# Kernel optimization log

Hardware: AMD Instinct MI355X
Metric: run time of the kernel (lower is better)

The kernel has to match this reference:

```python
import jax, jax.numpy as jnp
import numpy as np

B, C, H, W = 512, 256, 16, 16
K = H * W          # 256, hardcoded in the original reshape((1, 256))
N_CLASSES = 2      # binary private attribute
SIGMA = 1.0


def setup_inputs() -> dict:
    key = jax.random.key(0)
    k1, k2 = jax.random.split(key)
    mu = jax.random.normal(k1, (B, C, H, W), dtype=jnp.float32)
    private_attribute = jax.random.randint(k2, (B,), 0, N_CLASSES)
    cov = jnp.eye(K, dtype=jnp.float32) * SIGMA  # module buffer: eye(256) * sigma
    return {"mu": mu, "cov": cov, "private_attribute": private_attribute}


def reference(mu, cov, private_attribute):
    x = mu.reshape(B, C, K)                       # (B, C, 256)
    labels = private_attribute                    # (B,) int
    ones = jnp.ones((B,), x.dtype)
    counts = jax.ops.segment_sum(ones, labels, num_segments=N_CLASSES)        # (L,)
    safe = jnp.maximum(counts, 1.0)
    means = jax.ops.segment_sum(x, labels, num_segments=N_CLASSES) \
            / safe[:, None, None]                 # (L, C, K) per-label mean
    centered = x - means[labels]                  # (B, C, K) x_i - mu_{label(i)}
    onehot = (labels[:, None] == jnp.arange(N_CLASSES)[None, :]).astype(x.dtype)  # (B, L)
    # per-label scatter matrices: Sigma_l = sum_{i: label=l} (x_i-mu_l)^T (x_i-mu_l)
    S = jnp.stack([
        jnp.einsum('bci,bcj->cij', centered * onehot[:, l][:, None, None], centered)
        for l in range(N_CLASSES)
    ])                                            # (L, C, K, K)
    Sigma = cov[None, None] + S / safe[:, None, None, None]
    Sinv = jnp.linalg.inv(Sigma)                  # (L, C, K, K)
    _, logdet = jnp.linalg.slogdet(Sigma)         # (L, C)
    result = jnp.zeros((), x.dtype)
    # pairwise KL(N_i || N_j) with the original's asymmetric index pattern
    for i in range(N_CLASSES - 1):
        for j in range(1, N_CLASSES):
            if j == i:
                continue
            tr = jnp.einsum('cab,cba->c', Sinv[j], Sigma[i])         # trace(S2^{-1} S1)
            d = means[j] - means[i]                                  # (C, K)
            quad = jnp.einsum('ci,cij,cj->c', d, Sinv[j], d)
            kl = 0.5 * (tr + quad - K + logdet[j] - logdet[i])       # (C,)
            result = result + jnp.sum(kl) * counts[i] * counts[j]
    return result / C / (B ** 2)
```

## Files before the change

kernel.cpp:

```cpp
#include <hip/hip_runtime.h>
#include <cmath>

typedef __attribute__((ext_vector_type(4))) float f32x4;
typedef __attribute__((ext_vector_type(8))) short bf16x8;

#define MSZ 65536

__device__ __forceinline__ unsigned short f2bf(float f){
  unsigned u = __float_as_uint(f);
  unsigned r = (u + 0x7FFFu + ((u >> 16) & 1u)) >> 16;
  return (unsigned short)r;
}

__device__ __forceinline__ float dot4(f32x4 a, f32x4 b){
  return a.x*b.x + a.y*b.y + a.z*b.z + a.w*b.w;
}

__device__ __forceinline__ void tri_decode(int i, int& R, int& C){
  int Rv = (int)((sqrtf(8.f*(float)i + 1.f) - 1.f) * 0.5f);
  while ((Rv+1)*(Rv+2)/2 <= i) ++Rv;
  while (Rv*(Rv+1)/2 > i) --Rv;
  R = Rv; C = i - Rv*(Rv+1)/2;
}

__global__ void k_sentinel(float* __restrict__ out){ out[0] = 123456.0f; }

__global__ void k0_partition(const int* __restrict__ lab, int* __restrict__ cnt, int* __restrict__ idx){
  __shared__ int lcnt0[8], lcnt1[8];
  int t = threadIdx.x;
  int w = t >> 6, lane = t & 63;
  int l = lab[t];
  unsigned long long m0 = __ballot(l == 0);
  unsigned long long bm = (lane == 0) ? 0ull : ((1ull << lane) - 1ull);
  int r0 = __popcll(m0 & bm);
  int r1 = __popcll((~m0) & bm);
  if (lane == 0){ lcnt0[w] = __popcll(m0); lcnt1[w] = 64 - __popcll(m0); }
  __syncthreads();
  int base0 = 0, base1 = 0, n0 = 0;
  #pragma unroll
  for (int i = 0; i < 8; ++i){
    if (i < w){ base0 += lcnt0[i]; base1 += lcnt1[i]; }
    n0 += lcnt0[i];
  }
  int pos = (l == 0) ? (base0 + r0) : (n0 + base1 + r1);
  idx[pos] = t;
  if (t == 0){ cnt[0] = n0; cnt[1] = 512 - n0; }
}

__global__ __launch_bounds__(1024) void k1_means(const float* __restrict__ x, const int* __restrict__ lab,
                                                 const int* __restrict__ cnt, float* __restrict__ means){
  __shared__ int labs[512];
  __shared__ float part[8][256];
  int t = threadIdx.x, c = blockIdx.x;
  if (t < 512) labs[t] = lab[t];
  __syncthreads();
  int k = t & 255, bq = t >> 8;
  float s0 = 0.f, s1 = 0.f;
  const float* xc = x + (size_t)c * 256 + k;
  for (int b = bq; b < 512; b += 4){
    float v = xc[(size_t)b * 65536];
    if (labs[b] == 0) s0 += v; else s1 += v;
  }
  part[bq*2+0][k] = s0;
  part[bq*2+1][k] = s1;
  __syncthreads();
  if (t < 256){
    float m0 = part[0][t] + part[2][t] + part[4][t] + part[6][t];
    float m1 = part[1][t] + part[3][t] + part[5][t] + part[7][t];
    float n0 = (float)cnt[0], n1 = (float)cnt[1];
    means[(size_t)c * 256 + t]         = m0 / fmaxf(n0, 1.f);
    means[(size_t)(256 + c) * 256 + t] = m1 / fmaxf(n1, 1.f);
  }
}

__global__ __launch_bounds__(512) void k2_gram(const float* __restrict__ x, const float* __restrict__ cov,
    const float* __restrict__ means, const int* __restrict__ cnt, const int* __restrict__ idx,
    float* __restrict__ sig, int c0){
  __shared__ uint4 XT4[1280];
  __shared__ float mlds[256];
  int t = threadIdx.x;
  int bid = blockIdx.x;
  int l = bid & 1, c = c0 + (bid >> 1);
  int n0 = cnt[0], n1 = cnt[1];
  int n = l ? n1 : n0;
  int start = l ? n0 : 0;
  if (t < 256) mlds[t] = means[(size_t)(l * 256 + c) * 256 + t];

  f32x4 acc[8][4];
  #pragma unroll
  for (int i = 0; i < 8; ++i)
    #pragma unroll
    for (int jn = 0; jn < 4; ++jn){ f32x4 z; z.x = 0.f; z.y = 0.f; z.z = 0.f; z.w = 0.f; acc[i][jn] = z; }

  int lane = t & 63, wav = t >> 6;
  int wr = wav >> 2, wc = wav & 3;
  int lrow = lane & 15, lhalf = lane >> 4;
  int kq = t & 255, bh = t >> 8;
  int nst = (n + 31) >> 5;

  for (int s = 0; s < nst; ++s){
    __syncthreads();
    unsigned pk[8];
    #pragma unroll
    for (int m = 0; m < 8; ++m){
      int b0 = s * 32 + bh * 16 + 2 * m;
      float v0 = 0.f, v1 = 0.f;
      if (b0 < n)     v0 = x[((size_t)idx[start + b0] * 256 + c) * 256 + kq];
      if (b0 + 1 < n) v1 = x[((size_t)idx[start + b0 + 1] * 256 + c) * 256 + kq];
      pk[m] = (unsigned)f2bf(v0) | ((unsigned)f2bf(v1) << 16);
    }
    XT4[kq * 5 + bh * 2 + 0] = make_uint4(pk[0], pk[1], pk[2], pk[3]);
    XT4[kq * 5 + bh * 2 + 1] = make_uint4(pk[4], pk[5], pk[6], pk[7]);
    __syncthreads();
    bf16x8 af[8], bfr[4];
    #pragma unroll
    for (int i = 0; i < 8; ++i){
      int T = wr * 8 + i;
      af[i] = *reinterpret_cast<const bf16x8*>(&XT4[(T * 16 + lrow) * 5 + lhalf]);
    }
    #pragma unroll
    for (int jn = 0; jn < 4; ++jn){
      int T = wc * 4 + jn;
      bfr[jn] = *reinterpret_cast<const bf16x8*>(&XT4[(T * 16 + lrow) * 5 + lhalf]);
    }
    #pragma unroll
    for (int i = 0; i < 8; ++i)
      #pragma unroll
      for (int jn = 0; jn < 4; ++jn)
        acc[i][jn] = __builtin_amdgcn_mfma_f32_16x16x32_bf16(af[i], bfr[jn], acc[i][jn], 0, 0, 0);
  }
  __syncthreads();

  float invn = 1.0f / fmaxf((float)n, 1.0f);
  float* sigm = sig + (size_t)bid * MSZ;
  #pragma unroll
  for (int i = 0; i < 8; ++i){
    int Rb = (wr * 8 + i) * 16 + lhalf * 4;
    #pragma unroll
    for (int jn = 0; jn < 4; ++jn){
      int Cc = (wc * 4 + jn) * 16 + lrow;
      #pragma unroll
      for (int r = 0; r < 4; ++r){
        int R = Rb + r;
        float v = acc[i][jn][r] * invn + cov[R * 256 + Cc] - mlds[R] * mlds[Cc];
        sigm[R * 256 + Cc] = (Cc <= R) ? v : 0.0f;
      }
    }
  }
}

__device__ void factor128_v13(float* __restrict__ LB, int t, float& ldacc){
  for (int kb = 0; kb < 4; ++kb){
    int j0 = kb * 32;
    if (t < 64){
      #pragma unroll 1
      for (int s8 = 0; s8 < 8; ++s8){
        int js = j0 + 4*s8;
        float a00 = LB[(js+0)*132 + js+0];
        float a10 = LB[(js+1)*132 + js+0], a11 = LB[(js+1)*132 + js+1];
        float a20 = LB[(js+2)*132 + js+0], a21 = LB[(js+2)*132 + js+1], a22 = LB[(js+2)*132 + js+2];
        float a30 = LB[(js+3)*132 + js+0], a31 = LB[(js+3)*132 + js+1], a32 = LB[(js+3)*132 + js+2], a33 = LB[(js+3)*132 + js+3];
        float l00 = sqrtf(a00);
        float i00 = 1.0f / l00;
        float l10 = a10 * i00, l20 = a20 * i00, l30 = a30 * i00;
        float l11 = sqrtf(a11 - l10*l10);
        float i11 = 1.0f / l11;
        float l21 = (a21 - l20*l10) * i11, l31 = (a31 - l30*l10) * i11;
        float l22 = sqrtf(a22 - l20*l20 - l21*l21);
        float i22 = 1.0f / l22;
        float l32 = (a32 - l30*l20 - l31*l21) * i22;
        float l33 = sqrtf(a33 - l30*l30 - l31*l31 - l32*l32);
        float i33 = 1.0f / l33;
        if (t == 0){
          LB[(js+0)*132 + js+0] = l00;
          LB[(js+1)*132 + js+0] = l10; LB[(js+1)*132 + js+1] = l11;
          LB[(js+2)*132 + js+0] = l20; LB[(js+2)*132 + js+1] = l21; LB[(js+2)*132 + js+2] = l22;
          LB[(js+3)*132 + js+0] = l30; LB[(js+3)*132 + js+1] = l31; LB[(js+3)*132 + js+2] = l32; LB[(js+3)*132 + js+3] = l33;
          ldacc += logf(l00) + logf(l11) + logf(l22) + logf(l33);
        }
        int cnt2 = 28 - 4*s8;
        int r = js + 4 + t;
        if (t < cnt2){
          float w0 = LB[r*132 + js+0], w1 = LB[r*132 + js+1], w2 = LB[r*132 + js+2], w3 = LB[r*132 + js+3];
          w0 = w0 * i00;
          w1 = (w1 - l10*w0) * i11;
          w2 = (w2 - l20*w0 - l21*w1) * i22;
          w3 = (w3 - l30*w0 - l31*w1 - l32*w2) * i33;
          LB[r*132 + js+0] = w0; LB[r*132 + js+1] = w1; LB[r*132 + js+2] = w2; LB[r*132 + js+3] = w3;
          #pragma unroll 4
          for (int cq2 = js + 4; cq2 <= r; ++cq2){
            f32x4 Lc = *(const f32x4*)&LB[cq2*132 + js];
            LB[r*132 + cq2] -= w0*Lc.x + w1*Lc.y + w2*Lc.z + w3*Lc.w;
          }
        }
      }
    }
    __syncthreads();
    int nr = 96 - j0;
    if (nr > 0){
      if (t < nr){
        int row = j0 + 32 + t;
        float w[32];
        #pragma unroll
        for (int q = 0; q < 8; ++q){
          f32x4 v = *(const f32x4*)&LB[row*132 + j0 + 4*q];
          w[4*q] = v.x; w[4*q+1] = v.y; w[4*q+2] = v.z; w[4*q+3] = v.w;
        }
        #pragma unroll
        for (int cc = 0; cc < 32; ++cc){
          float s = w[cc];
          #pragma unroll
          for (int p = 0; p < cc; ++p) s -= LB[(j0+cc)*132 + j0 + p] * w[p];
          w[cc] = s / LB[(j0+cc)*132 + j0 + cc];
        }
        #pragma unroll
        for (int q = 0; q < 8; ++q){
          f32x4 v; v.x = w[4*q]; v.y = w[4*q+1]; v.z = w[4*q+2]; v.w = w[4*q+3];
          *(f32x4*)&LB[row*132 + j0 + 4*q] = v;
        }
      }
      __syncthreads();
      int nt = nr >> 2;
      int Tt = nt*(nt+1)/2;
      if (t < Tt){
        int R, C; tri_decode(t, R, C);
        int rb = j0+32+4*R, cb = j0+32+4*C;
        float s[16];
        #pragma unroll
        for (int q = 0; q < 16; ++q) s[q] = 0.f;
        #pragma unroll 4
        for (int qc = 0; qc < 8; ++qc){
          f32x4 a0 = *(const f32x4*)&LB[(rb+0)*132 + j0 + 4*qc];
          f32x4 a1 = *(const f32x4*)&LB[(rb+1)*132 + j0 + 4*qc];
          f32x4 a2 = *(const f32x4*)&LB[(rb+2)*132 + j0 + 4*qc];
          f32x4 a3 = *(const f32x4*)&LB[(rb+3)*132 + j0 + 4*qc];
          f32x4 b0 = *(const f32x4*)&LB[(cb+0)*132 + j0 + 4*qc];
          f32x4 b1 = *(const f32x4*)&LB[(cb+1)*132 + j0 + 4*qc];
          f32x4 b2 = *(const f32x4*)&LB[(cb+2)*132 + j0 + 4*qc];
          f32x4 b3 = *(const f32x4*)&LB[(cb+3)*132 + j0 + 4*qc];
          s[0]+=dot4(a0,b0);  s[1]+=dot4(a0,b1);  s[2]+=dot4(a0,b2);  s[3]+=dot4(a0,b3);
          s[4]+=dot4(a1,b0);  s[5]+=dot4(a1,b1);  s[6]+=dot4(a1,b2);  s[7]+=dot4(a1,b3);
          s[8]+=dot4(a2,b0);  s[9]+=dot4(a2,b1);  s[10]+=dot4(a2,b2); s[11]+=dot4(a2,b3);
          s[12]+=dot4(a3,b0); s[13]+=dot4(a3,b1); s[14]+=dot4(a3,b2); s[15]+=dot4(a3,b3);
        }
        #pragma unroll
        for (int i2 = 0; i2 < 4; ++i2)
          #pragma unroll
          for (int jl = 0; jl < 4; ++jl)
            LB[(rb+i2)*132 + cb+jl] -= s[i2*4+jl];
      }
    }
    __syncthreads();
  }
}

__global__ __launch_bounds__(512) void k3a_chol(float* __restrict__ sig, float* __restrict__ logdet, int c0){
  extern __shared__ float smem[];
  float* LB = smem;
  float* LT = smem + 16896;
  int t = threadIdx.x;
  int bid = blockIdx.x;
  int l = bid & 1, c = c0 + (bid >> 1);
  float* A = sig + (size_t)bid * MSZ;
  float ldacc = 0.f;

  for (int i = t; i < 4096; i += 512){
    int r = i >> 5, q = i & 31;
    *(f32x4*)&LB[r*132 + 4*q] = *(const f32x4*)&A[(size_t)r*256 + 4*q];
  }
  __syncthreads();
  factor128_v13(LB, t, ldacc);
  for (int i = t; i < 4096; i += 512){
    int r = i >> 5, q = i & 31;
    f32x4 v = *(const f32x4*)&LB[r*132 + 4*q];
    int cb = 4*q;
    v.x = (cb+0 <= r) ? v.x : 0.f;
    v.y = (cb+1 <= r) ? v.y : 0.f;
    v.z = (cb+2 <= r) ? v.z : 0.f;
    v.w = (cb+3 <= r) ? v.w : 0.f;
    *(f32x4*)&A[(size_t)r*256 + 4*q] = v;
  }
  __syncthreads();

  {
    int r2 = t >> 2, g = t & 3;
    for (int kb = 0; kb < 4; ++kb){
      f32x4 v0 = *(const f32x4*)&A[(size_t)(128+r2)*256 + 32*kb + 8*g];
      f32x4 v1 = *(const f32x4*)&A[(size_t)(128+r2)*256 + 32*kb + 8*g + 4];
      float accv[8] = {v0.x, v0.y, v0.z, v0.w, v1.x, v1.y, v1.z, v1.w};
      for (int p = 0; p < kb; ++p){
        __syncthreads();
        for (int i = t; i < 1024; i += 512){
          int j = i & 31, q = i >> 5;
          LT[q*33 + j] = A[(size_t)(32*kb + j)*256 + 32*p + q];
        }
        __syncthreads();
        f32x4 wv[8];
        #pragma unroll
        for (int q = 0; q < 8; ++q) wv[q] = *(const f32x4*)&LB[r2*132 + 32*p + 4*q];
        #pragma unroll
        for (int q4 = 0; q4 < 8; ++q4)
          #pragma unroll
          for (int jl = 0; jl < 8; ++jl)
            accv[jl] -= wv[q4].x * LT[(4*q4+0)*33 + 8*g+jl]
                      + wv[q4].y * LT[(4*q4+1)*33 + 8*g+jl]
                      + wv[q4].z * LT[(4*q4+2)*33 + 8*g+jl]
                      + wv[q4].w * LT[(4*q4+3)*33 + 8*g+jl];
      }
      #pragma unroll
      for (int jl = 0; jl < 8; ++jl) LB[r2*132 + 32*kb + 8*g + jl] = accv[jl];
      __syncthreads();
      for (int i = t; i < 1024; i += 512){
        int cc = i >> 5, p = i & 31;
        LT[cc*33 + p] = A[(size_t)(32*kb + cc)*256 + 32*kb + p];
      }
      __syncthreads();
      if (t < 128){
        float w[32];
        #pragma unroll
        for (int q = 0; q < 8; ++q){
          f32x4 v = *(const f32x4*)&LB[t*132 + 32*kb + 4*q];
          w[4*q] = v.x; w[4*q+1] = v.y; w[4*q+2] = v.z; w[4*q+3] = v.w;
        }
        #pragma unroll
        for (int cc = 0; cc < 32; ++cc){
          float s = w[cc];
          #pragma unroll
          for (int p = 0; p < cc; ++p) s -= LT[cc*33 + p] * w[p];
          w[cc] = s / LT[cc*33 + cc];
        }
        #pragma unroll
        for (int q = 0; q < 8; ++q){
          f32x4 v; v.x = w[4*q]; v.y = w[4*q+1]; v.z = w[4*q+2]; v.w = w[4*q+3];
          *(f32x4*)&LB[t*132 + 32*kb + 4*q] = v;
        }
      }
      __syncthreads();
    }
    for (int i = t; i < 4096; i += 512){
      int rr = i >> 5, q = i & 31;
      *(f32x4*)&A[(size_t)(128+rr)*256 + 4*q] = *(const f32x4*)&LB[rr*132 + 4*q];
    }
  }

  float s1[16], s2[16];
  int R1 = 0, C1 = 0, R2 = 0, C2 = 0;
  bool v1 = (t < 528), v2 = (t < 16);
  if (v1) tri_decode(t, R1, C1);
  if (v2) tri_decode(512 + t, R2, C2);
  #pragma unroll
  for (int q = 0; q < 16; ++q){ s1[q] = 0.f; s2[q] = 0.f; }
  if (v1){
    for (int qc = 0; qc < 32; ++qc){
      f32x4 a0 = *(const f32x4*)&LB[(4*R1+0)*132 + 4*qc];
      f32x4 a1 = *(const f32x4*)&LB[(4*R1+1)*132 + 4*qc];
      f32x4 a2 = *(const f32x4*)&LB[(4*R1+2)*132 + 4*qc];
      f32x4 a3 = *(const f32x4*)&LB[(4*R1+3)*132 + 4*qc];
      f32x4 b0 = *(const f32x4*)&LB[(4*C1+0)*132 + 4*qc];
      f32x4 b1 = *(const f32x4*)&LB[(4*C1+1)*132 + 4*qc];
      f32x4 b2 = *(const f32x4*)&LB[(4*C1+2)*132 + 4*qc];
      f32x4 b3 = *(const f32x4*)&LB[(4*C1+3)*132 + 4*qc];
      s1[0]+=dot4(a0,b0);  s1[1]+=dot4(a0,b1);  s1[2]+=dot4(a0,b2);  s1[3]+=dot4(a0,b3);
      s1[4]+=dot4(a1,b0);  s1[5]+=dot4(a1,b1);  s1[6]+=dot4(a1,b2);  s1[7]+=dot4(a1,b3);
      s1[8]+=dot4(a2,b0);  s1[9]+=dot4(a2,b1);  s1[10]+=dot4(a2,b2); s1[11]+=dot4(a2,b3);
      s1[12]+=dot4(a3,b0); s1[13]+=dot4(a3,b1); s1[14]+=dot4(a3,b2); s1[15]+=dot4(a3,b3);
    }
    #pragma unroll
    for (int i2 = 0; i2 < 4; ++i2){
      f32x4 av = *(const f32x4*)&A[(size_t)(128+4*R1+i2)*256 + 128 + 4*C1];
      s1[i2*4+0] = av.x - s1[i2*4+0];
      s1[i2*4+1] = av.y - s1[i2*4+1];
      s1[i2*4+2] = av.z - s1[i2*4+2];
      s1[i2*4+3] = av.w - s1[i2*4+3];
    }
  }
  if (v2){
    for (int qc = 0; qc < 32; ++qc){
      f32x4 a0 = *(const f32x4*)&LB[(4*R2+0)*132 + 4*qc];
      f32x4 a1 = *(const f32x4*)&LB[(4*R2+1)*132 + 4*qc];
      f32x4 a2 = *(const f32x4*)&LB[(4*R2+2)*132 + 4*qc];
      f32x4 a3 = *(const f32x4*)&LB[(4*R2+3)*132 + 4*qc];
      f32x4 b0 = *(const f32x4*)&LB[(4*C2+0)*132 + 4*qc];
      f32x4 b1 = *(const f32x4*)&LB[(4*C2+1)*132 + 4*qc];
      f32x4 b2 = *(const f32x4*)&LB[(4*C2+2)*132 + 4*qc];
      f32x4 b3 = *(const f32x4*)&LB[(4*C2+3)*132 + 4*qc];
      s2[0]+=dot4(a0,b0);  s2[1]+=dot4(a0,b1);  s2[2]+=dot4(a0,b2);  s2[3]+=dot4(a0,b3);
      s2[4]+=dot4(a1,b0);  s2[5]+=dot4(a1,b1);  s2[6]+=dot4(a1,b2);  s2[7]+=dot4(a1,b3);
      s2[8]+=dot4(a2,b0);  s2[9]+=dot4(a2,b1);  s2[10]+=dot4(a2,b2); s2[11]+=dot4(a2,b3);
      s2[12]+=dot4(a3,b0); s2[13]+=dot4(a3,b1); s2[14]+=dot4(a3,b2); s2[15]+=dot4(a3,b3);
    }
    #pragma unroll
    for (int i2 = 0; i2 < 4; ++i2){
      f32x4 av = *(const f32x4*)&A[(size_t)(128+4*R2+i2)*256 + 128 + 4*C2];
      s2[i2*4+0] = av.x - s2[i2*4+0];
      s2[i2*4+1] = av.y - s2[i2*4+1];
      s2[i2*4+2] = av.z - s2[i2*4+2];
      s2[i2*4+3] = av.w - s2[i2*4+3];
    }
  }
  __syncthreads();
  if (v1){
    #pragma unroll
    for (int i2 = 0; i2 < 4; ++i2)
      #pragma unroll
      for (int jl = 0; jl < 4; ++jl)
        LB[(4*R1+i2)*132 + 4*C1+jl] = s1[i2*4+jl];
  }
  if (v2){
    #pragma unroll
    for (int i2 = 0; i2 < 4; ++i2)
      #pragma unroll
      for (int jl = 0; jl < 4; ++jl)
        LB[(4*R2+i2)*132 + 4*C2+jl] = s2[i2*4+jl];
  }
  __syncthreads();

  factor128_v13(LB, t, ldacc);
  for (int i = t; i < 4096; i += 512){
    int r = i >> 5, q = i & 31;
    f32x4 v = *(const f32x4*)&LB[r*132 + 4*q];
    int cb = 4*q;
    v.x = (cb+0 <= r) ? v.x : 0.f;
    v.y = (cb+1 <= r) ? v.y : 0.f;
    v.z = (cb+2 <= r) ? v.z : 0.f;
    v.w = (cb+3 <= r) ? v.w : 0.f;
    *(f32x4*)&A[(size_t)(128+r)*256 + 128 + 4*q] = v;
  }
  if (t < 32){
    float v = ldacc;
    #pragma unroll
    for (int m = 1; m < 32; m <<= 1) v += __shfl_xor(v, m);
    if (t == 0) logdet[l * 256 + c] = 2.0f * v;
  }
}

__global__ __launch_bounds__(256) void k3b_trsm(float* __restrict__ sig, float* __restrict__ trp, int c0){
  __shared__ float L1blk[32 * 256];
  __shared__ float redw[4];
  int t = threadIdx.x, b = blockIdx.x;
  int lane = t & 63, wav = t >> 6;
  const float* L1 = sig + (size_t)(b * 2 + 1) * MSZ;
  float* W = sig + (size_t)(b * 2) * MSZ;
  float tracc = 0.f;

  for (int RB = 0; RB < 8; ++RB){
    int r0 = RB * 32;
    __syncthreads();
    for (int i = t; i < 32 * 256; i += 256)
      L1blk[i] = L1[(size_t)(r0 + (i >> 8)) * 256 + (i & 255)];
    __syncthreads();

    float acc[32];
    #pragma unroll
    for (int r = 0; r < 32; ++r) acc[r] = W[(size_t)(r0 + r) * 256 + t];

    for (int p = 0; p < r0; p += 8){
      float wv[8];
      #pragma unroll
      for (int q = 0; q < 8; ++q) wv[q] = W[(size_t)(p + q) * 256 + t];
      #pragma unroll
      for (int r = 0; r < 32; ++r){
        const f32x4 La = *(const f32x4*)&L1blk[r * 256 + p];
        const f32x4 Lb = *(const f32x4*)&L1blk[r * 256 + p + 4];
        acc[r] -= La.x * wv[0] + La.y * wv[1] + La.z * wv[2] + La.w * wv[3]
                + Lb.x * wv[4] + Lb.y * wv[5] + Lb.z * wv[6] + Lb.w * wv[7];
      }
    }
    #pragma unroll
    for (int rr = 0; rr < 32; ++rr){
      float v = acc[rr];
      #pragma unroll
      for (int q = 0; q < rr; ++q)
        v -= L1blk[rr * 256 + r0 + q] * acc[q];
      v /= L1blk[rr * 256 + r0 + rr];
      acc[rr] = v;
      tracc += v * v;
      W[(size_t)(r0 + rr) * 256 + t] = v;
    }
  }
  #pragma unroll
  for (int m = 1; m < 64; m <<= 1) tracc += __shfl_xor(tracc, m);
  if (lane == 0) redw[wav] = tracc;
  __syncthreads();
  if (t == 0) trp[c0 + b] = redw[0] + redw[1] + redw[2] + redw[3];
}

__global__ __launch_bounds__(64) void k3c_quad(const float* __restrict__ means, const float* __restrict__ sig,
    const float* __restrict__ trp, const float* __restrict__ logdet, float* __restrict__ klp, int c0){
  __shared__ float y[256];
  int t = threadIdx.x, b = blockIdx.x;
  int c = c0 + b;
  const float* L1 = sig + (size_t)(b * 2 + 1) * MSZ;
  const float* m1p = means + (size_t)(256 + c) * 256;
  const float* m0p = means + (size_t)c * 256;

  for (int r = 0; r < 256; ++r){
    float part = 0.f;
    for (int p = t; p < r; p += 64)
      part += L1[(size_t)r * 256 + p] * y[p];
    #pragma unroll
    for (int m = 1; m < 64; m <<= 1) part += __shfl_xor(part, m);
    if (t == 0)
      y[r] = ((m1p[r] - m0p[r]) - part) / L1[(size_t)r * 256 + r];
    __syncthreads();
  }
  float q = 0.f;
  #pragma unroll
  for (int i = 0; i < 4; ++i){ float v = y[t + 64 * i]; q += v * v; }
  #pragma unroll
  for (int m = 1; m < 64; m <<= 1) q += __shfl_xor(q, m);
  if (t == 0)
    klp[c] = 0.5f * (trp[c] + q - 256.0f + logdet[256 + c] - logdet[c]);
}

__global__ void k4_final(const float* __restrict__ klp, const int* __restrict__ cnt, float* __restrict__ out){
  __shared__ float red[256];
  int t = threadIdx.x;
  red[t] = klp[t];
  __syncthreads();
  for (int s = 128; s > 0; s >>= 1){
    if (t < s) red[t] += red[t + s];
    __syncthreads();
  }
  if (t == 0){
    float n0 = (float)cnt[0], n1 = (float)cnt[1];
    out[0] = red[0] * n0 * n1 / 256.0f / 512.0f / 512.0f;
  }
}

extern "C" void kernel_launch(void* const* d_in, const int* in_sizes, int n_in,
                              void* d_out, int out_size, void* d_ws, size_t ws_size,
                              hipStream_t stream){
  (void)in_sizes; (void)n_in; (void)out_size;
  const float* mu  = (const float*)d_in[0];
  const float* cov = (const float*)d_in[1];
  const int*   lab = (const int*)d_in[2];
  float* out = (float*)d_out;
  char* ws = (char*)d_ws;
  float* means  = (float*)ws;
  float* trp    = (float*)(ws + 524288);
  float* klp    = (float*)(ws + 525312);
  float* logdet = (float*)(ws + 526336);
  int*   cnt    = (int*)  (ws + 528384);
  int*   idx    = (int*)  (ws + 528392);
  float* sig    = (float*)(ws + 1048576);
  const size_t base = 1048576;

  int ch = 0;
  if      (ws_size >= base + (size_t)256 * 2 * MSZ * 4) ch = 256;
  else if (ws_size >= base + (size_t)64  * 2 * MSZ * 4) ch = 64;
  else if (ws_size >= base + (size_t)16  * 2 * MSZ * 4) ch = 16;
  else if (ws_size >= base + (size_t)4   * 2 * MSZ * 4) ch = 4;
  else if (ws_size >= base + (size_t)1   * 2 * MSZ * 4) ch = 1;
  if (ch == 0){
    k_sentinel<<<1, 1, 0, stream>>>(out);
    return;
  }

  const int k3a_lds = 17952 * 4;
  (void)hipFuncSetAttribute((const void*)k3a_chol,
                            hipFuncAttributeMaxDynamicSharedMemorySize, k3a_lds);

  k0_partition<<<1, 512, 0, stream>>>(lab, cnt, idx);
  k1_means<<<256, 1024, 0, stream>>>(mu, lab, cnt, means);
  for (int c0 = 0; c0 < 256; c0 += ch){
    k2_gram<<<ch * 2, 512, 0, stream>>>(mu, cov, means, cnt, idx, sig, c0);
    k3a_chol<<<ch * 2, 512, k3a_lds, stream>>>(sig, logdet, c0);
    k3b_trsm<<<ch, 256, 0, stream>>>(sig, trp, c0);
    k3c_quad<<<ch, 64, 0, stream>>>(means, sig, trp, logdet, klp, c0);
  }
  k4_final<<<1, 256, 0, stream>>>(klp, cnt, out);
}
```

Measured before the change: 1.109 ms.

## Fuse quadratic-form triangular solve into TRSM kernel using shared L blocks

Removes the separate k3c_quad kernel. Its forward substitution for the mean difference now runs in wave 0 of k3b_trsm, reusing the L1 row blocks already staged in LDS. The KL term per channel is then computed there. This drops one launch per chunk and the serial global-memory row reads of the old 64-thread quad kernel. In exchange, wave 0 does extra serial work inside each block step, which could lengthen the TRSM critical path.

New measurement: 929.3 us. -16.2%, faster.

```diff
diff --git a/kernel.cpp b/kernel.cpp
--- a/kernel.cpp
+++ b/kernel.cpp
@@ -434,21 +434,43 @@
   }
 }
 
-__global__ __launch_bounds__(256) void k3b_trsm(float* __restrict__ sig, float* __restrict__ trp, int c0){
+__global__ __launch_bounds__(256) void k3b_trsm(const float* __restrict__ means, float* __restrict__ sig,
+    const float* __restrict__ logdet, float* __restrict__ klp, int c0){
   __shared__ float L1blk[32 * 256];
-  __shared__ float redw[4];
+  __shared__ float yl[256];
+  __shared__ float dl[256];
+  __shared__ float redw[4], redq[4];
   int t = threadIdx.x, b = blockIdx.x;
+  int c = c0 + b;
   int lane = t & 63, wav = t >> 6;
   const float* L1 = sig + (size_t)(b * 2 + 1) * MSZ;
   float* W = sig + (size_t)(b * 2) * MSZ;
   float tracc = 0.f;
 
+  if (t < 256){
+    dl[t] = means[(size_t)(256 + c) * 256 + t] - means[(size_t)c * 256 + t];
+    yl[t] = 0.f;
+  }
+
   for (int RB = 0; RB < 8; ++RB){
     int r0 = RB * 32;
     __syncthreads();
     for (int i = t; i < 32 * 256; i += 256)
       L1blk[i] = L1[(size_t)(r0 + (i >> 8)) * 256 + (i & 255)];
     __syncthreads();
+
+    if (wav == 0){
+      for (int rr = 0; rr < 32; ++rr){
+        int r = r0 + rr;
+        const float* row = &L1blk[rr * 256];
+        float part = row[lane] * yl[lane] + row[lane + 64] * yl[lane + 64]
+                   + row[lane + 128] * yl[lane + 128] + row[lane + 192] * yl[lane + 192];
+        #pragma unroll
+        for (int m = 1; m < 64; m <<= 1) part += __shfl_xor(part, m);
+        float val = (dl[r] - part) / row[r];
+        if (lane == 0) yl[r] = val;
+      }
+    }
 
     float acc[32];
     #pragma unroll
@@ -478,39 +500,19 @@
       W[(size_t)(r0 + rr) * 256 + t] = v;
     }
   }
+  __syncthreads();
+  float qv = (t < 256) ? yl[t] * yl[t] : 0.f;
+  #pragma unroll
+  for (int m = 1; m < 64; m <<= 1) qv += __shfl_xor(qv, m);
   #pragma unroll
   for (int m = 1; m < 64; m <<= 1) tracc += __shfl_xor(tracc, m);
-  if (lane == 0) redw[wav] = tracc;
-  __syncthreads();
-  if (t == 0) trp[c0 + b] = redw[0] + redw[1] + redw[2] + redw[3];
-}
-
-__global__ __launch_bounds__(64) void k3c_quad(const float* __restrict__ means, const float* __restrict__ sig,
-    const float* __restrict__ trp, const float* __restrict__ logdet, float* __restrict__ klp, int c0){
-  __shared__ float y[256];
-  int t = threadIdx.x, b = blockIdx.x;
-  int c = c0 + b;
-  const float* L1 = sig + (size_t)(b * 2 + 1) * MSZ;
-  const float* m1p = means + (size_t)(256 + c) * 256;
-  const float* m0p = means + (size_t)c * 256;
-
-  for (int r = 0; r < 256; ++r){
-    float part = 0.f;
-    for (int p = t; p < r; p += 64)
-      part += L1[(size_t)r * 256 + p] * y[p];
-    #pragma unroll
-    for (int m = 1; m < 64; m <<= 1) part += __shfl_xor(part, m);
-    if (t == 0)
-      y[r] = ((m1p[r] - m0p[r]) - part) / L1[(size_t)r * 256 + r];
-    __syncthreads();
-  }
-  float q = 0.f;
-  #pragma unroll
-  for (int i = 0; i < 4; ++i){ float v = y[t + 64 * i]; q += v * v; }
-  #pragma unroll
-  for (int m = 1; m < 64; m <<= 1) q += __shfl_xor(q, m);
-  if (t == 0)
-    klp[c] = 0.5f * (trp[c] + q - 256.0f + logdet[256 + c] - logdet[c]);
+  if (lane == 0){ redw[wav] = tracc; redq[wav] = qv; }
+  __syncthreads();
+  if (t == 0){
+    float tr = redw[0] + redw[1] + redw[2] + redw[3];
+    float qq = redq[0] + redq[1] + redq[2] + redq[3];
+    klp[c] = 0.5f * (tr + qq - 256.0f + logdet[256 + c] - logdet[c]);
+  }
 }
 
 __global__ void k4_final(const float* __restrict__ klp, const int* __restrict__ cnt, float* __restrict__ out){
@@ -538,7 +540,6 @@
   float* out = (float*)d_out;
   char* ws = (char*)d_ws;
   float* means  = (float*)ws;
-  float* trp    = (float*)(ws + 524288);
   float* klp    = (float*)(ws + 525312);
   float* logdet = (float*)(ws + 526336);
   int*   cnt    = (int*)  (ws + 528384);
@@ -566,8 +567,7 @@
   for (int c0 = 0; c0 < 256; c0 += ch){
     k2_gram<<<ch * 2, 512, 0, stream>>>(mu, cov, means, cnt, idx, sig, c0);
     k3a_chol<<<ch * 2, 512, k3a_lds, stream>>>(sig, logdet, c0);
-    k3b_trsm<<<ch, 256, 0, stream>>>(sig, trp, c0);
-    k3c_quad<<<ch, 64, 0, stream>>>(means, sig, trp, logdet, klp, c0);
+    k3b_trsm<<<ch, 256, 0, stream>>>(means, sig, logdet, klp, c0);
   }
   k4_final<<<1, 256, 0, stream>>>(klp, cnt, out);
 }
```
